# Performance work log

Measured on AMD Instinct MI355X. Metric: run time of the kernel, lower is better.

## Reference

```python
import jax, jax.numpy as jnp
import numpy as np

RRELU_SLOPE = (1.0 / 8.0 + 1.0 / 3.0) / 2.0  # F.rrelu eval mode
N_ENT, N_REL2, H, E, B, T = 20000, 460, 128, 400000, 1024, 8


def _lin(x, W, b):
    return x @ W.T + b  # torch nn.Linear convention


def _gru_cell(x, h, w_ih, w_hh, b_ih, b_hh):
    gi = x @ w_ih.T + b_ih
    gh = h @ w_hh.T + b_hh
    i_r, i_z, i_n = jnp.split(gi, 3, axis=1)
    h_r, h_z, h_n = jnp.split(gh, 3, axis=1)
    r = jax.nn.sigmoid(i_r + h_r)
    z = jax.nn.sigmoid(i_z + h_z)
    n = jnp.tanh(i_n + r * h_n)
    return (1.0 - z) * n + z * h


def setup_inputs() -> dict:
    key = jax.random.key(0)
    ks = jax.random.split(key, 24)
    s = 0.02
    inp = {
        'ent_emb': jax.random.normal(ks[0], (N_ENT, H), jnp.float32),
        'rel_emb': jax.random.normal(ks[1], (N_REL2, H), jnp.float32),
        'weight_neighbor': jax.random.normal(ks[2], (H, H), jnp.float32) * s,
        'loop_weight': jax.random.normal(ks[3], (H, H), jnp.float32) * s,
        'evolve_loop_weight': jax.random.normal(ks[4], (H, H), jnp.float32) * s,
        'w_ih': jax.random.normal(ks[5], (3 * H, H), jnp.float32) * s,
        'w_hh': jax.random.normal(ks[6], (3 * H, H), jnp.float32) * s,
        'b_ih': jnp.zeros((3 * H,), jnp.float32),
        'b_hh': jnp.zeros((3 * H,), jnp.float32),
        'W_map1': jax.random.normal(ks[7], (2 * H, H), jnp.float32) * s,
        'b_map1': jnp.zeros((2 * H,), jnp.float32),
        'W_map2': jax.random.normal(ks[8], (H, 2 * H), jnp.float32) * s,
        'b_map2': jnp.zeros((H,), jnp.float32),
        'W_h1': jax.random.normal(ks[9], (H, H), jnp.float32) * s,
        'b_h1': jnp.zeros((H,), jnp.float32),
        'W_h2': jax.random.normal(ks[10], (H, H), jnp.float32) * s,
        'b_h2': jnp.zeros((H,), jnp.float32),
        'W_align': jax.random.normal(ks[11], (H, H), jnp.float32) * s,
        'b_align': jnp.zeros((H,), jnp.float32),
        'W_attn': jax.random.normal(ks[12], (H, H), jnp.float32) * s,
        'b_attn': jnp.zeros((H,), jnp.float32),
    }
    u = jax.random.uniform(ks[13], (B, T * N_REL2), jnp.float32)
    mask = jax.random.uniform(ks[14], (B, T * N_REL2)) > 0.7  # sparse history
    inp['partial_embeding'] = u * mask
    inp['edge_src'] = jax.random.randint(ks[15], (E,), 0, N_ENT, jnp.int32)
    inp['edge_dst'] = jax.random.randint(ks[16], (E,), 0, N_ENT, jnp.int32)
    inp['edge_type'] = jax.random.randint(ks[17], (E,), 0, N_REL2, jnp.int32)
    sub = jax.random.randint(ks[18], (B,), 0, N_ENT, jnp.int32)
    rel = jax.random.randint(ks[19], (B,), 0, N_REL2, jnp.int32)
    obj = jax.random.randint(ks[20], (B,), 0, N_ENT, jnp.int32)
    inp['triples'] = jnp.stack([sub, rel, obj], axis=1)
    return inp


def reference(ent_emb, rel_emb, weight_neighbor, loop_weight, evolve_loop_weight,
              w_ih, w_hh, b_ih, b_hh, W_map1, b_map1, W_map2, b_map2,
              W_h1, b_h1, W_h2, b_h2, W_align, b_align, W_attn, b_attn,
              partial_embeding, edge_src, edge_dst, edge_type, triples):
    # ---- UnionRGCNLayer: gather-transform-scatter ----
    h = ent_emb
    msg = (h[edge_src] + rel_emb[edge_type]) @ weight_neighbor          # [E, H]
    agg = jax.ops.segment_sum(msg, edge_dst, num_segments=N_ENT)        # [N, H]
    deg = jax.ops.segment_sum(jnp.ones((edge_dst.shape[0],), h.dtype), edge_dst,
                              num_segments=N_ENT)
    norm = jnp.where(deg > 0, 1.0 / jnp.where(deg > 0, deg, 1.0), 0.0)[:, None]
    loop = jnp.where((deg > 0)[:, None], h @ loop_weight, h @ evolve_loop_weight)
    x = agg * norm + loop
    pre_emb = jnp.where(x >= 0, x, x * RRELU_SLOPE)                     # rrelu (eval)

    # ---- PathPredictor.forward_back ----
    mapped_rel = _lin(_lin(rel_emb, W_map1, b_map1), W_map2, b_map2)    # [2R, H]
    q_rel = mapped_rel[triples[:, 1]]                                   # [B, H]
    A = _lin(q_rel, W_attn, b_attn) @ mapped_rel.T                      # [B, 2R]
    hist = partial_embeding.reshape(B, T, N_REL2).transpose(1, 0, 2)    # [T, B, 2R]

    def step(gh, cur):
        attn = cur * A
        attn = jax.nn.softmax(jnp.where(attn == 0, -1e9, attn), axis=1)
        rel_path = attn @ mapped_rel                                    # [B, H]
        return _gru_cell(rel_path, gh, w_ih, w_hh, b_ih, b_hh), None

    gru_hidden, _ = jax.lax.scan(step, jnp.zeros((B, H), pre_emb.dtype), hist)
    predicted_hist = 0.1 * _lin(_lin(q_rel, W_h1, b_h1), W_h2, b_h2) + q_rel
    match_loss = jnp.mean((predicted_hist - gru_hidden) ** 2)

    # ---- forward_forth, distmult scoring ----
    gh2 = _gru_cell(q_rel, predicted_hist, w_ih, w_hh, b_ih, b_hh)      # [B, H]
    sub_emb = pre_emb[triples[:, 0]]
    aligned_all = _lin(pre_emb, W_align, b_align)                       # [N, H]
    score_ = (_lin(sub_emb, W_align, b_align) * gh2) @ aligned_all.T    # [B, N]
    score = jax.nn.sigmoid(score_)
    # BCE(score, one_hot(obj)) without materializing labels:
    logp = jax.nn.log_sigmoid(score_)
    log1mp = jax.nn.log_sigmoid(-score_)
    total = -jnp.sum(log1mp)
    rows = jnp.arange(B)
    total = total + jnp.sum(log1mp[rows, triples[:, 2]] - logp[rows, triples[:, 2]])
    path_loss = total / (B * N_ENT)
    return score, match_loss, path_loss
```

## Files before the change

kernel.cpp:

```cpp
#include <hip/hip_runtime.h>

typedef unsigned short u16;
typedef unsigned int u32;
typedef __attribute__((ext_vector_type(8))) short bf8v;
typedef __attribute__((ext_vector_type(4))) float f4v;

#define RRELU_SLOPE 0.22916666667f

__device__ inline float bf2f(u16 u){ unsigned int i = ((unsigned int)u) << 16; float f; __builtin_memcpy(&f, &i, 4); return f; }
__device__ inline u16 f2bf(float f){ unsigned int i; __builtin_memcpy(&i, &f, 4); unsigned int r = (i + 0x7fffu + ((i >> 16) & 1u)) >> 16; return (u16)r; }
__device__ inline float frcp(float x){ return __builtin_amdgcn_rcpf(x); }
__device__ inline float fsigm(float x){ return frcp(1.f + __expf(-x)); }
__device__ inline float ftanh(float x){ return 2.f * frcp(1.f + __expf(-2.f * x)) - 1.f; }

__global__ __launch_bounds__(256) void prep_k(
    const float* __restrict__ Wn, const float* __restrict__ Wl, const float* __restrict__ We,
    const float* __restrict__ wih, const float* __restrict__ whh,
    const float* __restrict__ m1, const float* __restrict__ m2,
    const float* __restrict__ h1, const float* __restrict__ h2,
    const float* __restrict__ attn, const float* __restrict__ alg, const float* __restrict__ rel,
    const float* __restrict__ ent, const float* __restrict__ bat, const float* __restrict__ bh1,
    u16* __restrict__ Bcat, u16* __restrict__ wihb, u16* __restrict__ whhb,
    u16* __restrict__ m1b, u16* __restrict__ m2b, u16* __restrict__ h1b, u16* __restrict__ h2b,
    u16* __restrict__ attnb, u16* __restrict__ algb, u16* __restrict__ relb,
    u16* __restrict__ entb, float* __restrict__ bias2)
{
    int id = blockIdx.x * 256 + threadIdx.x;
    if (id < 49152) {
        int n = id / 384, k = id % 384;
        float v = (k < 128) ? Wn[k*128 + n] : (k < 256 ? Wl[(k-128)*128 + n] : We[(k-256)*128 + n]);
        Bcat[id] = f2bf(v); return;
    }
    id -= 49152;
    if (id < 49152) { wihb[id] = f2bf(wih[id]); return; } id -= 49152;
    if (id < 49152) { whhb[id] = f2bf(whh[id]); return; } id -= 49152;
    if (id < 32768) { m1b[id]  = f2bf(m1[id]);  return; } id -= 32768;
    if (id < 32768) { m2b[id]  = f2bf(m2[id]);  return; } id -= 32768;
    if (id < 16384) { h1b[id]  = f2bf(h1[id]);  return; } id -= 16384;
    if (id < 16384) { h2b[id]  = f2bf(h2[id]);  return; } id -= 16384;
    if (id < 16384) { attnb[id]= f2bf(attn[id]);return; } id -= 16384;
    if (id < 16384) { algb[id] = f2bf(alg[id]); return; } id -= 16384;
    if (id < 58880) { relb[id] = f2bf(rel[id]); return; } id -= 58880;
    if (id < 2560000) { entb[id] = f2bf(ent[id]); return; } id -= 2560000;
    if (id < 256) { bias2[id] = (id < 128) ? bat[id] : bh1[id - 128]; }
}

__global__ __launch_bounds__(256) void hist_k(
    const int* __restrict__ dst, int* __restrict__ hist, int E)
{
    int e = blockIdx.x * 256 + threadIdx.x;
    if (e < E) atomicAdd(&hist[dst[e]], 1);
}

__global__ __launch_bounds__(1024) void scan_k(
    const int* __restrict__ hist, int* __restrict__ starts, int* __restrict__ cursor)
{
    __shared__ int part[1024];
    int t = threadIdx.x;
    int base = t * 20;
    int s = 0;
    for (int j = 0; j < 20; ++j) { int idx = base + j; if (idx < 20000) s += hist[idx]; }
    part[t] = s;
    __syncthreads();
    for (int off = 1; off < 1024; off <<= 1) {
        int v = (t >= off) ? part[t - off] : 0;
        __syncthreads();
        part[t] += v;
        __syncthreads();
    }
    int run = (t > 0) ? part[t - 1] : 0;
    for (int j = 0; j < 20; ++j) {
        int idx = base + j;
        if (idx < 20000) { starts[idx] = run; cursor[idx] = run; run += hist[idx]; }
    }
    if (t == 1023) starts[20000] = run;
}

__global__ __launch_bounds__(256) void scatter_k(
    const int* __restrict__ src, const int* __restrict__ dst, const int* __restrict__ typ,
    int* __restrict__ cursor, int2* __restrict__ spack, int E)
{
    int e = blockIdx.x * 256 + threadIdx.x;
    if (e >= E) return;
    int d = dst[e];
    int p = atomicAdd(&cursor[d], 1);
    spack[p] = make_int2(src[e], typ[e]);
}

__global__ __launch_bounds__(64) void agg_acat_k(
    const int2* __restrict__ spack, const int* __restrict__ starts,
    const u32* __restrict__ hb, const u32* __restrict__ rb, u32* __restrict__ Acat32)
{
    int i = blockIdx.x;
    int lane = threadIdx.x;
    int s0 = starts[i], s1 = starts[i + 1];
    float sx = 0.f, sy = 0.f;
    int e = s0;
    for (; e + 4 <= s1; e += 4) {
        int2 st0 = spack[e], st1 = spack[e+1], st2 = spack[e+2], st3 = spack[e+3];
        u32 a0 = hb[(long)st0.x * 64 + lane]; u32 r0 = rb[(long)st0.y * 64 + lane];
        u32 a1 = hb[(long)st1.x * 64 + lane]; u32 r1 = rb[(long)st1.y * 64 + lane];
        u32 a2 = hb[(long)st2.x * 64 + lane]; u32 r2 = rb[(long)st2.y * 64 + lane];
        u32 a3 = hb[(long)st3.x * 64 + lane]; u32 r3 = rb[(long)st3.y * 64 + lane];
        sx += bf2f((u16)(a0 & 0xffff)) + bf2f((u16)(r0 & 0xffff));
        sy += bf2f((u16)(a0 >> 16))    + bf2f((u16)(r0 >> 16));
        sx += bf2f((u16)(a1 & 0xffff)) + bf2f((u16)(r1 & 0xffff));
        sy += bf2f((u16)(a1 >> 16))    + bf2f((u16)(r1 >> 16));
        sx += bf2f((u16)(a2 & 0xffff)) + bf2f((u16)(r2 & 0xffff));
        sy += bf2f((u16)(a2 >> 16))    + bf2f((u16)(r2 >> 16));
        sx += bf2f((u16)(a3 & 0xffff)) + bf2f((u16)(r3 & 0xffff));
        sy += bf2f((u16)(a3 >> 16))    + bf2f((u16)(r3 >> 16));
    }
    for (; e < s1; ++e) {
        int2 st = spack[e];
        u32 a = hb[(long)st.x * 64 + lane];
        u32 r = rb[(long)st.y * 64 + lane];
        sx += bf2f((u16)(a & 0xffff)) + bf2f((u16)(r & 0xffff));
        sy += bf2f((u16)(a >> 16))    + bf2f((u16)(r >> 16));
    }
    bool has = s1 > s0;
    float nrm = has ? frcp((float)(s1 - s0)) : 0.f;
    u32 hv = hb[(long)i * 64 + lane];
    u32 agg = (u32)f2bf(sx * nrm) | ((u32)f2bf(sy * nrm) << 16);
    long o = (long)i * 192 + lane;
    Acat32[o]       = agg;
    Acat32[o + 64]  = has ? hv : 0u;
    Acat32[o + 128] = has ? 0u : hv;
}

__global__ __launch_bounds__(256) void gemm_nt(
    const u16* __restrict__ A, const u16* __restrict__ B, const float* __restrict__ bias,
    float* __restrict__ Cf, u16* __restrict__ Cbf, u16* __restrict__ CT,
    const u16* __restrict__ residb, const int* __restrict__ arows,
    int M, int N, int K, int lda, int ldb, int ldc, int ldct, int arow_stride,
    float rscale, int epi)
{
    int tid = threadIdx.x;
    int wave = tid >> 6, lane = tid & 63;
    int ln = lane & 15, q = lane >> 4;
    int bm = blockIdx.y * 64 + wave * 16;
    int bn = blockIdx.x * 64;
    int am = bm + ln; if (am >= M) am = M - 1;
    long ar = arows ? (long)arows[(long)am * arow_stride] : (long)am;
    const u16* Ap = A + ar * lda;
    int br[4];
#pragma unroll
    for (int nt = 0; nt < 4; ++nt) { int n = bn + nt*16 + ln; br[nt] = (n < N) ? n : (N - 1); }
    f4v acc[4] = {};
    for (int kc = 0; kc < K; kc += 32) {
        bf8v af = *(const bf8v*)(Ap + kc + q*8);
#pragma unroll
        for (int nt = 0; nt < 4; ++nt) {
            bf8v bv = *(const bf8v*)(B + (long)br[nt]*ldb + kc + q*8);
            acc[nt] = __builtin_amdgcn_mfma_f32_16x16x32_bf16(af, bv, acc[nt], 0, 0, 0);
        }
    }
#pragma unroll
    for (int nt = 0; nt < 4; ++nt) {
        int n = bn + nt*16 + ln;
        if (n >= N) continue;
        float bv = bias ? bias[n] : 0.f;
#pragma unroll
        for (int r = 0; r < 4; ++r) {
            int m = bm + q*4 + r;
            if (m >= M) continue;
            float v = acc[nt][r] + bv;
            if (epi == 1) v = (v >= 0.f) ? v : v * RRELU_SLOPE;
            if (residb)  v = rscale * v + bf2f(residb[(long)m*ldc + n]);
            long ci = (long)m*ldc + n;
            if (Cf)  Cf[ci]  = v;
            if (Cbf) Cbf[ci] = f2bf(v);
            if (CT)  CT[(long)n*ldct + m] = f2bf(v);
        }
    }
}

__global__ __launch_bounds__(256) void fuse_map_k(
    const u16* __restrict__ relb, const u16* __restrict__ m1b, const float* __restrict__ bm1,
    const u16* __restrict__ m2b, const float* __restrict__ bm2,
    u16* __restrict__ mapb, u16* __restrict__ mapT)
{
    __shared__ u16 t1l[4][16][264];
    int tid = threadIdx.x;
    int wave = tid >> 6, lane = tid & 63;
    int ln = lane & 15, q = lane >> 4;
    int base = blockIdx.x * 64 + wave * 16;
    int arow = base + ln; if (arow > 459) arow = 459;
    const u16* Ap = relb + arow * 128;
    f4v acc1[16] = {};
    for (int kc = 0; kc < 128; kc += 32) {
        bf8v af = *(const bf8v*)(Ap + kc + q*8);
#pragma unroll
        for (int nt = 0; nt < 16; ++nt) {
            bf8v bv = *(const bf8v*)(m1b + (nt*16 + ln)*128 + kc + q*8);
            acc1[nt] = __builtin_amdgcn_mfma_f32_16x16x32_bf16(af, bv, acc1[nt], 0, 0, 0);
        }
    }
#pragma unroll
    for (int nt = 0; nt < 16; ++nt) {
        int n = nt*16 + ln;
        float bv = bm1[n];
#pragma unroll
        for (int r = 0; r < 4; ++r)
            t1l[wave][q*4 + r][n] = f2bf(acc1[nt][r] + bv);
    }
    f4v acc2[8] = {};
    for (int kc = 0; kc < 256; kc += 32) {
        bf8v af = *(const bf8v*)&t1l[wave][ln][kc + q*8];
#pragma unroll
        for (int nt = 0; nt < 8; ++nt) {
            bf8v bv = *(const bf8v*)(m2b + (nt*16 + ln)*256 + kc + q*8);
            acc2[nt] = __builtin_amdgcn_mfma_f32_16x16x32_bf16(af, bv, acc2[nt], 0, 0, 0);
        }
    }
#pragma unroll
    for (int nt = 0; nt < 8; ++nt) {
        int n = nt*16 + ln;
        float bv = bm2[n];
#pragma unroll
        for (int r = 0; r < 4; ++r) {
            int m = base + q*4 + r;
            if (m < 460) {
                u16 hv = f2bf(acc2[nt][r] + bv);
                mapb[m*128 + n] = hv;
                mapT[n*480 + m] = hv;
            }
        }
    }
}

__global__ __launch_bounds__(256) void qrel_k(
    const u16* __restrict__ mapb, const int* __restrict__ trip,
    u16* __restrict__ qrelb, u16* __restrict__ X)
{
    int id = blockIdx.x * 256 + threadIdx.x;
    int b = id >> 7, k = id & 127;
    int r = trip[b*3 + 1];
    u16 v = mapb[r*128 + k];
    qrelb[id] = v;
    X[(long)(8192 + b)*128 + k] = v;
}

__global__ __launch_bounds__(256) void fuse_qt_k(
    const u16* __restrict__ qrelb, const u16* __restrict__ atb, const float* __restrict__ bias2,
    const u16* __restrict__ h2b, const float* __restrict__ bh2,
    u16* __restrict__ atq, float* __restrict__ pred)
{
    __shared__ u16 th1l[4][16][136];
    int tid = threadIdx.x;
    int wave = tid >> 6, lane = tid & 63;
    int ln = lane & 15, q = lane >> 4;
    int base = blockIdx.x * 64 + wave * 16;
    const u16* Ap = qrelb + (base + ln) * 128;
    f4v acc1[16] = {};
    for (int kc = 0; kc < 128; kc += 32) {
        bf8v af = *(const bf8v*)(Ap + kc + q*8);
#pragma unroll
        for (int nt = 0; nt < 16; ++nt) {
            bf8v bv = *(const bf8v*)(atb + (nt*16 + ln)*128 + kc + q*8);
            acc1[nt] = __builtin_amdgcn_mfma_f32_16x16x32_bf16(af, bv, acc1[nt], 0, 0, 0);
        }
    }
#pragma unroll
    for (int nt = 0; nt < 16; ++nt) {
        int n = nt*16 + ln;
        float bv = bias2[n];
#pragma unroll
        for (int r = 0; r < 4; ++r) {
            float x = acc1[nt][r] + bv;
            if (nt < 8) atq[(base + q*4 + r)*128 + n] = f2bf(x);
            else        th1l[wave][q*4 + r][n - 128] = f2bf(x);
        }
    }
    f4v acc2[8] = {};
    for (int kc = 0; kc < 128; kc += 32) {
        bf8v af = *(const bf8v*)&th1l[wave][ln][kc + q*8];
#pragma unroll
        for (int nt = 0; nt < 8; ++nt) {
            bf8v bv = *(const bf8v*)(h2b + (nt*16 + ln)*128 + kc + q*8);
            acc2[nt] = __builtin_amdgcn_mfma_f32_16x16x32_bf16(af, bv, acc2[nt], 0, 0, 0);
        }
    }
#pragma unroll
    for (int nt = 0; nt < 8; ++nt) {
        int n = nt*16 + ln;
        float bv = bh2[n];
#pragma unroll
        for (int r = 0; r < 4; ++r) {
            int m = base + q*4 + r;
            pred[(long)m*128 + n] = 0.1f * (acc2[nt][r] + bv) + bf2f(qrelb[(long)m*128 + n]);
        }
    }
}

__global__ __launch_bounds__(256) void smrp_k(
    const float* __restrict__ Amat, const float* __restrict__ part,
    const u16* __restrict__ mapT, u16* __restrict__ X)
{
    __shared__ u16 xls[32][488];
    int tid = threadIdx.x;
    int wave = tid >> 6, lane = tid & 63;
    int base = blockIdx.x * 32;
    int t = base >> 10, b0 = base & 1023;
    for (int j = 0; j < 8; ++j) {
        int rl = wave*8 + j;
        int b = b0 + rl;
        const float* arow = Amat + (long)b*460;
        const float* crow = part + (long)b*3680 + t*460;
        float v[8], e[8];
        float m = -1e30f;
#pragma unroll
        for (int i = 0; i < 8; ++i) {
            int r = i*64 + lane;
            if (r < 460) {
                float x = crow[r] * arow[r];
                x = (x == 0.f) ? -1e9f : x;
                v[i] = x; m = fmaxf(m, x);
            } else v[i] = -1e30f;
        }
#pragma unroll
        for (int off = 32; off; off >>= 1) m = fmaxf(m, __shfl_xor(m, off));
        float sum = 0.f;
#pragma unroll
        for (int i = 0; i < 8; ++i) {
            int r = i*64 + lane;
            e[i] = 0.f;
            if (r < 460) { e[i] = __expf(v[i] - m); sum += e[i]; }
        }
#pragma unroll
        for (int off = 32; off; off >>= 1) sum += __shfl_xor(sum, off);
        float inv = frcp(sum);
#pragma unroll
        for (int i = 0; i < 8; ++i) {
            int r = i*64 + lane;
            if (r < 460)      xls[rl][r] = f2bf(e[i] * inv);
            else if (r < 488) xls[rl][r] = 0;
        }
    }
    __syncthreads();
    int ln = lane & 15, q = lane >> 4;
    f4v acc[2][2] = {};
    for (int kc = 0; kc < 480; kc += 32) {
        bf8v a[2], bfr[2];
#pragma unroll
        for (int mt = 0; mt < 2; ++mt)
            a[mt] = *(const bf8v*)&xls[mt*16 + ln][kc + q*8];
#pragma unroll
        for (int nt = 0; nt < 2; ++nt)
            bfr[nt] = *(const bf8v*)(mapT + (wave*32 + nt*16 + ln)*480 + kc + q*8);
#pragma unroll
        for (int mt = 0; mt < 2; ++mt)
#pragma unroll
            for (int nt = 0; nt < 2; ++nt)
                acc[mt][nt] = __builtin_amdgcn_mfma_f32_16x16x32_bf16(a[mt], bfr[nt], acc[mt][nt], 0, 0, 0);
    }
#pragma unroll
    for (int mt = 0; mt < 2; ++mt)
#pragma unroll
    for (int nt = 0; nt < 2; ++nt) {
        int n = wave*32 + nt*16 + ln;
#pragma unroll
        for (int r = 0; r < 4; ++r) {
            int m = base + mt*16 + q*4 + r;
            X[(long)m*128 + n] = f2bf(acc[mt][nt][r]);
        }
    }
}

__global__ __launch_bounds__(256) void gru_k(
    const float* __restrict__ gi, const u16* __restrict__ whhb, const float* __restrict__ bhh,
    const float* __restrict__ pred, float* __restrict__ gh2, float* __restrict__ match_acc)
{
    __shared__ u16  hbf[16][136];
    __shared__ float hf [4][128];
    __shared__ float ghl[4][388];
    __shared__ float red[4];
    int tid = threadIdx.x;
    int wave = tid >> 6, lane = tid & 63;
    int ln = lane & 15, q = lane >> 4;
    int bb = blockIdx.x * 4;
    for (int i = tid; i < 16*136; i += 256) hbf[i/136][i%136] = 0;
    for (int i = tid; i < 4*128; i += 256) hf[i>>7][i&127] = 0.f;
    bf8v bfrag[6][4];
#pragma unroll
    for (int nt = 0; nt < 6; ++nt)
#pragma unroll
        for (int kc = 0; kc < 4; ++kc)
            bfrag[nt][kc] = *(const bf8v*)(whhb + (long)(wave*96 + nt*16 + ln)*128 + kc*32 + q*8);
    int k = tid & 127;
    float br = bhh[k], bz = bhh[128 + k], bn_ = bhh[256 + k];
    __syncthreads();
    float msum = 0.f;
    for (int t = 0; t <= 8; ++t) {
        float gr[2], gz[2], gn[2], pv[2];
        long girow0 = (t < 8) ? ((long)t*1024 + bb) : (8192 + bb);
#pragma unroll
        for (int it = 0; it < 2; ++it) {
            int m = it*2 + (tid >> 7);
            const float* gp = gi + (girow0 + m)*384;
            gr[it] = gp[k]; gz[it] = gp[128 + k]; gn[it] = gp[256 + k];
            pv[it] = (t >= 7) ? pred[(long)(bb + m)*128 + k] : 0.f;
        }
        if (t == 8) {
#pragma unroll
            for (int it = 0; it < 2; ++it) {
                int m = it*2 + (tid >> 7);
                hf[m][k] = pv[it]; hbf[m][k] = f2bf(pv[it]);
            }
            __syncthreads();
        }
        f4v acc[6] = {};
#pragma unroll
        for (int kc = 0; kc < 4; ++kc) {
            bf8v af = *(const bf8v*)&hbf[ln][kc*32 + q*8];
#pragma unroll
            for (int nt = 0; nt < 6; ++nt)
                acc[nt] = __builtin_amdgcn_mfma_f32_16x16x32_bf16(af, bfrag[nt][kc], acc[nt], 0, 0, 0);
        }
        if (q == 0) {
#pragma unroll
            for (int nt = 0; nt < 6; ++nt)
#pragma unroll
                for (int r = 0; r < 4; ++r)
                    ghl[r][wave*96 + nt*16 + ln] = acc[nt][r];
        }
        __syncthreads();
#pragma unroll
        for (int it = 0; it < 2; ++it) {
            int m = it*2 + (tid >> 7);
            float rr = fsigm(gr[it] + ghl[m][k] + br);
            float zz = fsigm(gz[it] + ghl[m][128 + k] + bz);
            float nn = ftanh(gn[it] + rr * (ghl[m][256 + k] + bn_));
            float hn = (1.f - zz) * nn + zz * hf[m][k];
            if (t == 7) { float d = pv[it] - hn; msum += d*d; }
            if (t == 8) { gh2[(long)(bb + m)*128 + k] = hn; }
            else        { hf[m][k] = hn; hbf[m][k] = f2bf(hn); }
        }
        __syncthreads();
    }
#pragma unroll
    for (int off = 32; off; off >>= 1) msum += __shfl_down(msum, off);
    if (lane == 0) red[wave] = msum;
    __syncthreads();
    if (tid == 0) atomicAdd(match_acc, red[0] + red[1] + red[2] + red[3]);
}

__global__ __launch_bounds__(128) void vo_k(
    const float* __restrict__ subl, const float* __restrict__ gh2,
    const u16* __restrict__ AL, const int* __restrict__ trip,
    u16* __restrict__ V, float* __restrict__ obj_acc)
{
    int b = blockIdx.x, k = threadIdx.x;
    u16 vb = f2bf(subl[b*128 + k] * gh2[b*128 + k]);
    V[b*128 + k] = vb;
    int obj = trip[b*3 + 2];
    float s = bf2f(vb) * bf2f(AL[(long)obj*128 + k]);
#pragma unroll
    for (int off = 32; off; off >>= 1) s += __shfl_down(s, off);
    __shared__ float red2[2];
    if ((k & 63) == 0) red2[k >> 6] = s;
    __syncthreads();
    if (k == 0) atomicAdd(obj_acc, -(red2[0] + red2[1]));
}

__global__ __launch_bounds__(512) void score_k(
    const u16* __restrict__ V, const u16* __restrict__ AL,
    float* __restrict__ out, float* __restrict__ sp_acc, int N)
{
    __shared__ float stage[8][2048];
    int tid = threadIdx.x;
    int wave = tid >> 6, lane = tid & 63;
    int ln = lane & 15, q = lane >> 4;
    int bm = blockIdx.y * 128 + (wave >> 2) * 64;
    int bn = blockIdx.x * 128 + (wave & 3) * 32;
    bool valid = bn < N;
    int br[2];
#pragma unroll
    for (int nt = 0; nt < 2; ++nt) { int n = bn + nt*16 + ln; br[nt] = (n < N) ? n : (N - 1); }
    f4v acc[4][2] = {};
    for (int kc = 0; kc < 128; kc += 32) {
        bf8v a[4], b[2];
#pragma unroll
        for (int mt = 0; mt < 4; ++mt)
            a[mt] = *(const bf8v*)(V + (long)(bm + mt*16 + ln)*128 + kc + q*8);
#pragma unroll
        for (int nt = 0; nt < 2; ++nt)
            b[nt] = *(const bf8v*)(AL + (long)br[nt]*128 + kc + q*8);
#pragma unroll
        for (int mt = 0; mt < 4; ++mt)
#pragma unroll
            for (int nt = 0; nt < 2; ++nt)
                acc[mt][nt] = __builtin_amdgcn_mfma_f32_16x16x32_bf16(a[mt], b[nt], acc[mt][nt], 0, 0, 0);
    }
    float lsum = 0.f;
    float* st = stage[wave];
#pragma unroll
    for (int mt = 0; mt < 4; ++mt)
#pragma unroll
    for (int nt = 0; nt < 2; ++nt)
#pragma unroll
    for (int r = 0; r < 4; ++r) {
        float s = acc[mt][nt][r];
        float e = __expf(-fabsf(s));
        float d = 1.f + e;
        float inv = frcp(d);
        st[(mt*16 + q*4 + r)*32 + nt*16 + ln] = (s >= 0.f) ? inv : e * inv;
        lsum += fmaxf(s, 0.f) + __logf(d);
    }
    if (!valid) lsum = 0.f;
    if (valid) {
        int row0 = lane >> 3, c4 = (lane & 7) << 2;
#pragma unroll
        for (int i = 0; i < 8; ++i) {
            int row = i*8 + row0;
            f4v vv = *(const f4v*)&st[row*32 + c4];
            __builtin_nontemporal_store(vv, (f4v*)&out[(long)(bm + row)*N + bn + c4]);
        }
    }
#pragma unroll
    for (int off = 32; off; off >>= 1) lsum += __shfl_xor(lsum, off);
    __shared__ float red[8];
    if (lane == 0) red[wave] = lsum;
    __syncthreads();
    if (tid == 0) {
        float tsum = 0.f;
#pragma unroll
        for (int w = 0; w < 8; ++w) tsum += red[w];
        atomicAdd(sp_acc, tsum);
    }
}

__global__ void final_k(const float* __restrict__ acc, float* __restrict__ out)
{
    out[20480000] = acc[0] / (1024.f * 128.f);
    out[20480001] = (acc[1] + acc[2]) / (1024.f * 20000.f);
}

extern "C" void kernel_launch(void* const* d_in, const int* in_sizes, int n_in,
                              void* d_out, int out_size, void* d_ws, size_t ws_size,
                              hipStream_t stream)
{
    const float* ent  = (const float*)d_in[0];
    const float* rel  = (const float*)d_in[1];
    const float* Wn   = (const float*)d_in[2];
    const float* Wl   = (const float*)d_in[3];
    const float* We   = (const float*)d_in[4];
    const float* wih  = (const float*)d_in[5];
    const float* whh  = (const float*)d_in[6];
    const float* b_ih = (const float*)d_in[7];
    const float* b_hh = (const float*)d_in[8];
    const float* Wm1  = (const float*)d_in[9];
    const float* bm1  = (const float*)d_in[10];
    const float* Wm2  = (const float*)d_in[11];
    const float* bm2  = (const float*)d_in[12];
    const float* Wh1  = (const float*)d_in[13];
    const float* bh1  = (const float*)d_in[14];
    const float* Wh2  = (const float*)d_in[15];
    const float* bh2  = (const float*)d_in[16];
    const float* Wal  = (const float*)d_in[17];
    const float* bal  = (const float*)d_in[18];
    const float* Wat  = (const float*)d_in[19];
    const float* bat  = (const float*)d_in[20];
    const float* part = (const float*)d_in[21];
    const int* esrc   = (const int*)d_in[22];
    const int* edst   = (const int*)d_in[23];
    const int* etyp   = (const int*)d_in[24];
    const int* trip   = (const int*)d_in[25];
    float* out = (float*)d_out;
    const int E = in_sizes[22];

    char* ws = (char*)d_ws;
    size_t off = 0;
    auto alloc = [&](size_t bytes) { size_t o = off; off = (off + bytes + 255) & ~(size_t)255; return o; };

    size_t o_acc   = alloc(256);
    size_t o_hist  = alloc(20000 * 4);
    size_t o_mapT  = alloc(128 * 480 * 2);
    size_t zend = off;
    size_t o_starts= alloc(20004 * 4);
    size_t o_cur   = alloc(20000 * 4);
    size_t o_spack = alloc((size_t)E * 8);
    size_t o_entb  = alloc((size_t)20000 * 128 * 2);
    size_t o_acat  = alloc((size_t)20000 * 384 * 2);
    size_t o_pre   = alloc((size_t)20000 * 128 * 2);
    size_t o_aln   = alloc((size_t)20000 * 128 * 2);
    size_t o_bcat  = alloc(128 * 384 * 2);
    size_t o_wih   = alloc(384 * 128 * 2);
    size_t o_whh   = alloc(384 * 128 * 2);
    size_t o_m1    = alloc(256 * 128 * 2);
    size_t o_m2    = alloc(128 * 256 * 2);
    size_t o_ath   = alloc(2 * 128 * 128 * 2);
    size_t o_h2    = alloc(128 * 128 * 2);
    size_t o_al    = alloc(128 * 128 * 2);
    size_t o_rel   = alloc(460 * 128 * 2);
    size_t o_map   = alloc(460 * 128 * 2);
    size_t o_qrel  = alloc(1024 * 128 * 2);
    size_t o_atq   = alloc(1024 * 128 * 2);
    size_t o_b2    = alloc(256 * 4);
    size_t o_pred  = alloc(1024 * 128 * 4);
    size_t o_amat  = alloc((size_t)1024 * 460 * 4);
    size_t o_X     = alloc((size_t)9216 * 128 * 2);
    size_t o_gi    = alloc((size_t)9216 * 384 * 4);
    size_t o_subl  = alloc(1024 * 128 * 4);
    size_t o_gh2   = alloc(1024 * 128 * 4);
    size_t o_V     = alloc(1024 * 128 * 2);

    float* accp  = (float*)(ws + o_acc);
    int* histp   = (int*)(ws + o_hist);
    u16* mapT    = (u16*)(ws + o_mapT);
    int* startsp = (int*)(ws + o_starts);
    int* curp    = (int*)(ws + o_cur);
    int2* spack  = (int2*)(ws + o_spack);
    u16* entb    = (u16*)(ws + o_entb);
    u16* acat    = (u16*)(ws + o_acat);
    u16* preb    = (u16*)(ws + o_pre);
    u16* alnb    = (u16*)(ws + o_aln);
    u16* bcat    = (u16*)(ws + o_bcat);
    u16* wihb    = (u16*)(ws + o_wih);
    u16* whhb    = (u16*)(ws + o_whh);
    u16* m1b     = (u16*)(ws + o_m1);
    u16* m2b     = (u16*)(ws + o_m2);
    u16* atb     = (u16*)(ws + o_ath);
    u16* h1b     = atb + 128 * 128;
    u16* h2b     = (u16*)(ws + o_h2);
    u16* alb     = (u16*)(ws + o_al);
    u16* relb    = (u16*)(ws + o_rel);
    u16* mapb    = (u16*)(ws + o_map);
    u16* qrelb   = (u16*)(ws + o_qrel);
    u16* atqb    = (u16*)(ws + o_atq);
    float* bias2 = (float*)(ws + o_b2);
    float* predf = (float*)(ws + o_pred);
    float* amat  = (float*)(ws + o_amat);
    u16* Xb      = (u16*)(ws + o_X);
    float* gif   = (float*)(ws + o_gi);
    float* subl  = (float*)(ws + o_subl);
    float* gh2f  = (float*)(ws + o_gh2);
    u16* Vb      = (u16*)(ws + o_V);

    hipMemsetAsync(ws, 0, zend, stream);

    prep_k<<<11319, 256, 0, stream>>>(Wn, Wl, We, wih, whh, Wm1, Wm2, Wh1, Wh2, Wat, Wal, rel,
                                      ent, bat, bh1,
                                      bcat, wihb, whhb, m1b, m2b, h1b, h2b, atb, alb, relb,
                                      entb, bias2);

    int eb = (E + 255) / 256;
    hist_k<<<eb, 256, 0, stream>>>(edst, histp, E);
    scan_k<<<1, 1024, 0, stream>>>(histp, startsp, curp);
    scatter_k<<<eb, 256, 0, stream>>>(esrc, edst, etyp, curp, spack, E);
    agg_acat_k<<<20000, 64, 0, stream>>>(spack, startsp, (const u32*)entb, (const u32*)relb, (u32*)acat);

    gemm_nt<<<dim3(2, 313), 256, 0, stream>>>(acat, bcat, nullptr, nullptr, preb, nullptr, nullptr, nullptr,
                                              20000, 128, 384, 384, 384, 128, 0, 0, 0.f, 1);
    gemm_nt<<<dim3(2, 313), 256, 0, stream>>>(preb, alb, bal, nullptr, alnb, nullptr, nullptr, nullptr,
                                              20000, 128, 128, 128, 128, 128, 0, 0, 0.f, 0);

    fuse_map_k<<<8, 256, 0, stream>>>(relb, m1b, bm1, m2b, bm2, mapb, mapT);

    qrel_k<<<512, 256, 0, stream>>>(mapb, trip, qrelb, Xb);

    fuse_qt_k<<<16, 256, 0, stream>>>(qrelb, atb, bias2, h2b, bh2, atqb, predf);

    gemm_nt<<<dim3(8, 16), 256, 0, stream>>>(atqb, mapb, nullptr, amat, nullptr, nullptr, nullptr, nullptr,
                                             1024, 460, 128, 128, 128, 460, 0, 0, 0.f, 0);

    smrp_k<<<256, 256, 0, stream>>>(amat, part, mapT, Xb);

    gemm_nt<<<dim3(6, 144), 256, 0, stream>>>(Xb, wihb, b_ih, gif, nullptr, nullptr, nullptr, nullptr,
                                              9216, 384, 128, 128, 128, 384, 0, 0, 0.f, 0);
    gemm_nt<<<dim3(2, 16), 256, 0, stream>>>(preb, alb, bal, subl, nullptr, nullptr, nullptr, trip,
                                             1024, 128, 128, 128, 128, 128, 0, 3, 0.f, 0);

    gru_k<<<256, 256, 0, stream>>>(gif, whhb, b_hh, predf, gh2f, accp + 0);

    vo_k<<<1024, 128, 0, stream>>>(subl, gh2f, alnb, trip, Vb, accp + 2);

    score_k<<<dim3(157, 8), 512, 0, stream>>>(Vb, alnb, out, accp + 1, 20000);

    final_k<<<1, 1, 0, stream>>>(accp, out);

    (void)in_sizes; (void)n_in; (void)out_size; (void)ws_size;
}
```

Measured before the change: 470.1 us.

## Fuse input-gate GEMM, vo and final into GRU; merge small kernels

Computes the GRU input projection inside the recurrent kernel from the bf16 X rows using register-resident W_ih fragments. This removes the 9216x384 fp32 gi buffer and its separate GEMM. The vo and final reductions are folded into gru_k and into score_k through a last-block counter, the histogram moves into prep_k, and qrel_k is folded into fuse_qt_k. smrp_k is regrouped so each block stages four Amat rows in shared memory across all timesteps. The cost is more registers and MFMA work on the serial GRU path, plus occupancy limited to one block per SM.

```diff
diff --git a/kernel.cpp b/kernel.cpp
--- a/kernel.cpp
+++ b/kernel.cpp
@@ -20,10 +20,11 @@
     const float* __restrict__ h1, const float* __restrict__ h2,
     const float* __restrict__ attn, const float* __restrict__ alg, const float* __restrict__ rel,
     const float* __restrict__ ent, const float* __restrict__ bat, const float* __restrict__ bh1,
+    const int* __restrict__ edst, int E,
     u16* __restrict__ Bcat, u16* __restrict__ wihb, u16* __restrict__ whhb,
     u16* __restrict__ m1b, u16* __restrict__ m2b, u16* __restrict__ h1b, u16* __restrict__ h2b,
     u16* __restrict__ attnb, u16* __restrict__ algb, u16* __restrict__ relb,
-    u16* __restrict__ entb, float* __restrict__ bias2)
+    u16* __restrict__ entb, float* __restrict__ bias2, int* __restrict__ hist)
 {
     int id = blockIdx.x * 256 + threadIdx.x;
     if (id < 49152) {
@@ -42,14 +43,8 @@
     if (id < 16384) { algb[id] = f2bf(alg[id]); return; } id -= 16384;
     if (id < 58880) { relb[id] = f2bf(rel[id]); return; } id -= 58880;
     if (id < 2560000) { entb[id] = f2bf(ent[id]); return; } id -= 2560000;
-    if (id < 256) { bias2[id] = (id < 128) ? bat[id] : bh1[id - 128]; }
-}
-
-__global__ __launch_bounds__(256) void hist_k(
-    const int* __restrict__ dst, int* __restrict__ hist, int E)
-{
-    int e = blockIdx.x * 256 + threadIdx.x;
-    if (e < E) atomicAdd(&hist[dst[e]], 1);
+    if (id < 256) { bias2[id] = (id < 128) ? bat[id] : bh1[id - 128]; return; } id -= 256;
+    if (id < E) atomicAdd(&hist[edst[id]], 1);
 }
 
 __global__ __launch_bounds__(1024) void scan_k(
@@ -229,29 +224,22 @@
     }
 }
 
-__global__ __launch_bounds__(256) void qrel_k(
+__global__ __launch_bounds__(256) void fuse_qt_k(
     const u16* __restrict__ mapb, const int* __restrict__ trip,
-    u16* __restrict__ qrelb, u16* __restrict__ X)
-{
-    int id = blockIdx.x * 256 + threadIdx.x;
-    int b = id >> 7, k = id & 127;
-    int r = trip[b*3 + 1];
-    u16 v = mapb[r*128 + k];
-    qrelb[id] = v;
-    X[(long)(8192 + b)*128 + k] = v;
-}
-
-__global__ __launch_bounds__(256) void fuse_qt_k(
-    const u16* __restrict__ qrelb, const u16* __restrict__ atb, const float* __restrict__ bias2,
+    const u16* __restrict__ atb, const float* __restrict__ bias2,
     const u16* __restrict__ h2b, const float* __restrict__ bh2,
-    u16* __restrict__ atq, float* __restrict__ pred)
+    u16* __restrict__ atq, float* __restrict__ pred, u16* __restrict__ X)
 {
     __shared__ u16 th1l[4][16][136];
     int tid = threadIdx.x;
     int wave = tid >> 6, lane = tid & 63;
     int ln = lane & 15, q = lane >> 4;
     int base = blockIdx.x * 64 + wave * 16;
-    const u16* Ap = qrelb + (base + ln) * 128;
+    int ar = trip[(base + ln)*3 + 1];
+    const u16* Ap = mapb + ar * 128;
+    int rm_[4];
+#pragma unroll
+    for (int r = 0; r < 4; ++r) rm_[r] = trip[(base + q*4 + r)*3 + 1];
     f4v acc1[16] = {};
     for (int kc = 0; kc < 128; kc += 32) {
         bf8v af = *(const bf8v*)(Ap + kc + q*8);
@@ -267,9 +255,12 @@
         float bv = bias2[n];
 #pragma unroll
         for (int r = 0; r < 4; ++r) {
+            int m = base + q*4 + r;
             float x = acc1[nt][r] + bv;
-            if (nt < 8) atq[(base + q*4 + r)*128 + n] = f2bf(x);
-            else        th1l[wave][q*4 + r][n - 128] = f2bf(x);
+            if (nt < 8) {
+                atq[m*128 + n] = f2bf(x);
+                X[(long)(8192 + m)*128 + n] = mapb[rm_[r]*128 + n];
+            } else th1l[wave][q*4 + r][n - 128] = f2bf(x);
         }
     }
     f4v acc2[8] = {};
@@ -288,7 +279,7 @@
 #pragma unroll
         for (int r = 0; r < 4; ++r) {
             int m = base + q*4 + r;
-            pred[(long)m*128 + n] = 0.1f * (acc2[nt][r] + bv) + bf2f(qrelb[(long)m*128 + n]);
+            pred[(long)m*128 + n] = 0.1f * (acc2[nt][r] + bv) + bf2f(mapb[rm_[r]*128 + n]);
         }
     }
 }
@@ -298,22 +289,24 @@
     const u16* __restrict__ mapT, u16* __restrict__ X)
 {
     __shared__ u16 xls[32][488];
+    __shared__ float asl[4][464];
     int tid = threadIdx.x;
     int wave = tid >> 6, lane = tid & 63;
-    int base = blockIdx.x * 32;
-    int t = base >> 10, b0 = base & 1023;
+    int b0 = blockIdx.x * 4;
+    for (int i = tid; i < 4*460; i += 256)
+        asl[i/460][i%460] = Amat[(long)(b0 + i/460)*460 + i%460];
+    __syncthreads();
     for (int j = 0; j < 8; ++j) {
         int rl = wave*8 + j;
-        int b = b0 + rl;
-        const float* arow = Amat + (long)b*460;
-        const float* crow = part + (long)b*3680 + t*460;
+        int t = rl >> 2, db = rl & 3;
+        const float* crow = part + (long)(b0 + db)*3680 + t*460;
         float v[8], e[8];
         float m = -1e30f;
 #pragma unroll
         for (int i = 0; i < 8; ++i) {
             int r = i*64 + lane;
             if (r < 460) {
-                float x = crow[r] * arow[r];
+                float x = crow[r] * asl[db][r];
                 x = (x == 0.f) ? -1e9f : x;
                 v[i] = x; m = fmaxf(m, x);
             } else v[i] = -1e30f;
@@ -361,44 +354,50 @@
         int n = wave*32 + nt*16 + ln;
 #pragma unroll
         for (int r = 0; r < 4; ++r) {
-            int m = base + mt*16 + q*4 + r;
-            X[(long)m*128 + n] = f2bf(acc[mt][nt][r]);
-        }
-    }
-}
-
-__global__ __launch_bounds__(256) void gru_k(
-    const float* __restrict__ gi, const u16* __restrict__ whhb, const float* __restrict__ bhh,
-    const float* __restrict__ pred, float* __restrict__ gh2, float* __restrict__ match_acc)
+            int rl = mt*16 + q*4 + r;
+            long m = (long)(rl >> 2)*1024 + b0 + (rl & 3);
+            X[m*128 + n] = f2bf(acc[mt][nt][r]);
+        }
+    }
+}
+
+__global__ __launch_bounds__(256, 1) void gru_k(
+    const u16* __restrict__ X, const u16* __restrict__ wihb, const float* __restrict__ bih,
+    const u16* __restrict__ whhb, const float* __restrict__ bhh,
+    const float* __restrict__ pred, const float* __restrict__ subl,
+    const u16* __restrict__ AL, const int* __restrict__ trip,
+    u16* __restrict__ V, float* __restrict__ accp)
 {
     __shared__ u16  hbf[16][136];
     __shared__ float hf [4][128];
     __shared__ float ghl[4][388];
-    __shared__ float red[4];
+    __shared__ float gil[4][388];
+    __shared__ float redm[4], redo[4];
     int tid = threadIdx.x;
     int wave = tid >> 6, lane = tid & 63;
     int ln = lane & 15, q = lane >> 4;
     int bb = blockIdx.x * 4;
     for (int i = tid; i < 16*136; i += 256) hbf[i/136][i%136] = 0;
     for (int i = tid; i < 4*128; i += 256) hf[i>>7][i&127] = 0.f;
-    bf8v bfrag[6][4];
+    bf8v bfrag[6][4], wfrag[6][4];
 #pragma unroll
     for (int nt = 0; nt < 6; ++nt)
 #pragma unroll
-        for (int kc = 0; kc < 4; ++kc)
+        for (int kc = 0; kc < 4; ++kc) {
             bfrag[nt][kc] = *(const bf8v*)(whhb + (long)(wave*96 + nt*16 + ln)*128 + kc*32 + q*8);
+            wfrag[nt][kc] = *(const bf8v*)(wihb + (long)(wave*96 + nt*16 + ln)*128 + kc*32 + q*8);
+        }
     int k = tid & 127;
-    float br = bhh[k], bz = bhh[128 + k], bn_ = bhh[256 + k];
+    float cr = bih[k] + bhh[k];
+    float cz = bih[128 + k] + bhh[128 + k];
+    float bin_ = bih[256 + k], bhn = bhh[256 + k];
     __syncthreads();
-    float msum = 0.f;
+    float msum = 0.f, osum = 0.f;
     for (int t = 0; t <= 8; ++t) {
-        float gr[2], gz[2], gn[2], pv[2];
-        long girow0 = (t < 8) ? ((long)t*1024 + bb) : (8192 + bb);
+        float pv[2];
 #pragma unroll
         for (int it = 0; it < 2; ++it) {
             int m = it*2 + (tid >> 7);
-            const float* gp = gi + (girow0 + m)*384;
-            gr[it] = gp[k]; gz[it] = gp[128 + k]; gn[it] = gp[256 + k];
             pv[it] = (t >= 7) ? pred[(long)(bb + m)*128 + k] : 0.f;
         }
         if (t == 8) {
@@ -409,63 +408,60 @@
             }
             __syncthreads();
         }
+        long xr0 = (t < 8) ? ((long)t*1024 + bb) : (long)(8192 + bb);
+        const u16* Xp = X + (xr0 + (ln & 3))*128;
+        f4v gacc[6] = {};
         f4v acc[6] = {};
 #pragma unroll
         for (int kc = 0; kc < 4; ++kc) {
+            bf8v xf = *(const bf8v*)(Xp + kc*32 + q*8);
             bf8v af = *(const bf8v*)&hbf[ln][kc*32 + q*8];
 #pragma unroll
+            for (int nt = 0; nt < 6; ++nt) {
+                gacc[nt] = __builtin_amdgcn_mfma_f32_16x16x32_bf16(xf, wfrag[nt][kc], gacc[nt], 0, 0, 0);
+                acc[nt]  = __builtin_amdgcn_mfma_f32_16x16x32_bf16(af, bfrag[nt][kc], acc[nt],  0, 0, 0);
+            }
+        }
+        if (q == 0) {
+#pragma unroll
             for (int nt = 0; nt < 6; ++nt)
-                acc[nt] = __builtin_amdgcn_mfma_f32_16x16x32_bf16(af, bfrag[nt][kc], acc[nt], 0, 0, 0);
-        }
-        if (q == 0) {
-#pragma unroll
-            for (int nt = 0; nt < 6; ++nt)
-#pragma unroll
-                for (int r = 0; r < 4; ++r)
+#pragma unroll
+                for (int r = 0; r < 4; ++r) {
                     ghl[r][wave*96 + nt*16 + ln] = acc[nt][r];
+                    gil[r][wave*96 + nt*16 + ln] = gacc[nt][r];
+                }
         }
         __syncthreads();
 #pragma unroll
         for (int it = 0; it < 2; ++it) {
             int m = it*2 + (tid >> 7);
-            float rr = fsigm(gr[it] + ghl[m][k] + br);
-            float zz = fsigm(gz[it] + ghl[m][128 + k] + bz);
-            float nn = ftanh(gn[it] + rr * (ghl[m][256 + k] + bn_));
+            float rr = fsigm(gil[m][k] + ghl[m][k] + cr);
+            float zz = fsigm(gil[m][128 + k] + ghl[m][128 + k] + cz);
+            float nn = ftanh(gil[m][256 + k] + bin_ + rr * (ghl[m][256 + k] + bhn));
             float hn = (1.f - zz) * nn + zz * hf[m][k];
             if (t == 7) { float d = pv[it] - hn; msum += d*d; }
-            if (t == 8) { gh2[(long)(bb + m)*128 + k] = hn; }
-            else        { hf[m][k] = hn; hbf[m][k] = f2bf(hn); }
+            if (t == 8) {
+                u16 vb = f2bf(subl[(long)(bb + m)*128 + k] * hn);
+                V[(long)(bb + m)*128 + k] = vb;
+                int obj = trip[(bb + m)*3 + 2];
+                osum += bf2f(vb) * bf2f(AL[(long)obj*128 + k]);
+            } else { hf[m][k] = hn; hbf[m][k] = f2bf(hn); }
         }
         __syncthreads();
     }
 #pragma unroll
-    for (int off = 32; off; off >>= 1) msum += __shfl_down(msum, off);
-    if (lane == 0) red[wave] = msum;
+    for (int off = 32; off; off >>= 1) { msum += __shfl_down(msum, off); osum += __shfl_down(osum, off); }
+    if (lane == 0) { redm[wave] = msum; redo[wave] = osum; }
     __syncthreads();
-    if (tid == 0) atomicAdd(match_acc, red[0] + red[1] + red[2] + red[3]);
-}
-
-__global__ __launch_bounds__(128) void vo_k(
-    const float* __restrict__ subl, const float* __restrict__ gh2,
-    const u16* __restrict__ AL, const int* __restrict__ trip,
-    u16* __restrict__ V, float* __restrict__ obj_acc)
-{
-    int b = blockIdx.x, k = threadIdx.x;
-    u16 vb = f2bf(subl[b*128 + k] * gh2[b*128 + k]);
-    V[b*128 + k] = vb;
-    int obj = trip[b*3 + 2];
-    float s = bf2f(vb) * bf2f(AL[(long)obj*128 + k]);
-#pragma unroll
-    for (int off = 32; off; off >>= 1) s += __shfl_down(s, off);
-    __shared__ float red2[2];
-    if ((k & 63) == 0) red2[k >> 6] = s;
-    __syncthreads();
-    if (k == 0) atomicAdd(obj_acc, -(red2[0] + red2[1]));
+    if (tid == 0) {
+        atomicAdd(accp + 0, redm[0] + redm[1] + redm[2] + redm[3]);
+        atomicAdd(accp + 2, -(redo[0] + redo[1] + redo[2] + redo[3]));
+    }
 }
 
 __global__ __launch_bounds__(512) void score_k(
     const u16* __restrict__ V, const u16* __restrict__ AL,
-    float* __restrict__ out, float* __restrict__ sp_acc, int N)
+    float* __restrict__ out, float* __restrict__ accp, int N)
 {
     __shared__ float stage[8][2048];
     int tid = threadIdx.x;
@@ -526,14 +522,18 @@
         float tsum = 0.f;
 #pragma unroll
         for (int w = 0; w < 8; ++w) tsum += red[w];
-        atomicAdd(sp_acc, tsum);
-    }
-}
-
-__global__ void final_k(const float* __restrict__ acc, float* __restrict__ out)
-{
-    out[20480000] = acc[0] / (1024.f * 128.f);
-    out[20480001] = (acc[1] + acc[2]) / (1024.f * 20000.f);
+        atomicAdd(accp + 1, tsum);
+        __threadfence();
+        u32* cnt = (u32*)accp + 3;
+        u32 c = atomicAdd(cnt, 1u);
+        if (c == gridDim.x * gridDim.y - 1) {
+            float mm = atomicAdd(accp + 0, 0.f);
+            float sp = atomicAdd(accp + 1, 0.f);
+            float ob = atomicAdd(accp + 2, 0.f);
+            out[20480000] = mm / (1024.f * 128.f);
+            out[20480001] = (sp + ob) / (1024.f * 20000.f);
+        }
+    }
 }
 
 extern "C" void kernel_launch(void* const* d_in, const int* in_sizes, int n_in,
@@ -594,15 +594,12 @@
     size_t o_al    = alloc(128 * 128 * 2);
     size_t o_rel   = alloc(460 * 128 * 2);
     size_t o_map   = alloc(460 * 128 * 2);
-    size_t o_qrel  = alloc(1024 * 128 * 2);
     size_t o_atq   = alloc(1024 * 128 * 2);
     size_t o_b2    = alloc(256 * 4);
     size_t o_pred  = alloc(1024 * 128 * 4);
     size_t o_amat  = alloc((size_t)1024 * 460 * 4);
     size_t o_X     = alloc((size_t)9216 * 128 * 2);
-    size_t o_gi    = alloc((size_t)9216 * 384 * 4);
     size_t o_subl  = alloc(1024 * 128 * 4);
-    size_t o_gh2   = alloc(1024 * 128 * 4);
     size_t o_V     = alloc(1024 * 128 * 2);
 
     float* accp  = (float*)(ws + o_acc);
@@ -626,27 +623,25 @@
     u16* alb     = (u16*)(ws + o_al);
     u16* relb    = (u16*)(ws + o_rel);
     u16* mapb    = (u16*)(ws + o_map);
-    u16* qrelb   = (u16*)(ws + o_qrel);
     u16* atqb    = (u16*)(ws + o_atq);
     float* bias2 = (float*)(ws + o_b2);
     float* predf = (float*)(ws + o_pred);
     float* amat  = (float*)(ws + o_amat);
     u16* Xb      = (u16*)(ws + o_X);
-    float* gif   = (float*)(ws + o_gi);
     float* subl  = (float*)(ws + o_subl);
-    float* gh2f  = (float*)(ws + o_gh2);
     u16* Vb      = (u16*)(ws + o_V);
 
     hipMemsetAsync(ws, 0, zend, stream);
 
-    prep_k<<<11319, 256, 0, stream>>>(Wn, Wl, We, wih, whh, Wm1, Wm2, Wh1, Wh2, Wat, Wal, rel,
-                                      ent, bat, bh1,
-                                      bcat, wihb, whhb, m1b, m2b, h1b, h2b, atb, alb, relb,
-                                      entb, bias2);
-
+    int ptot = 2897664 + E;
+    prep_k<<<(ptot + 255) / 256, 256, 0, stream>>>(
+        Wn, Wl, We, wih, whh, Wm1, Wm2, Wh1, Wh2, Wat, Wal, rel,
+        ent, bat, bh1, edst, E,
+        bcat, wihb, whhb, m1b, m2b, h1b, h2b, atb, alb, relb,
+        entb, bias2, histp);
+
+    scan_k<<<1, 1024, 0, stream>>>(histp, startsp, curp);
     int eb = (E + 255) / 256;
-    hist_k<<<eb, 256, 0, stream>>>(edst, histp, E);
-    scan_k<<<1, 1024, 0, stream>>>(histp, startsp, curp);
     scatter_k<<<eb, 256, 0, stream>>>(esrc, edst, etyp, curp, spack, E);
     agg_acat_k<<<20000, 64, 0, stream>>>(spack, startsp, (const u32*)entb, (const u32*)relb, (u32*)acat);
 
@@ -657,27 +652,19 @@
 
     fuse_map_k<<<8, 256, 0, stream>>>(relb, m1b, bm1, m2b, bm2, mapb, mapT);
 
-    qrel_k<<<512, 256, 0, stream>>>(mapb, trip, qrelb, Xb);
-
-    fuse_qt_k<<<16, 256, 0, stream>>>(qrelb, atb, bias2, h2b, bh2, atqb, predf);
+    fuse_qt_k<<<16, 256, 0, stream>>>(mapb, trip, atb, bias2, h2b, bh2, atqb, predf, Xb);
 
     gemm_nt<<<dim3(8, 16), 256, 0, stream>>>(atqb, mapb, nullptr, amat, nullptr, nullptr, nullptr, nullptr,
                                              1024, 460, 128, 128, 128, 460, 0, 0, 0.f, 0);
 
     smrp_k<<<256, 256, 0, stream>>>(amat, part, mapT, Xb);
 
-    gemm_nt<<<dim3(6, 144), 256, 0, stream>>>(Xb, wihb, b_ih, gif, nullptr, nullptr, nullptr, nullptr,
-                                              9216, 384, 128, 128, 128, 384, 0, 0, 0.f, 0);
     gemm_nt<<<dim3(2, 16), 256, 0, stream>>>(preb, alb, bal, subl, nullptr, nullptr, nullptr, trip,
                                              1024, 128, 128, 128, 128, 128, 0, 3, 0.f, 0);
 
-    gru_k<<<256, 256, 0, stream>>>(gif, whhb, b_hh, predf, gh2f, accp + 0);
-
-    vo_k<<<1024, 128, 0, stream>>>(subl, gh2f, alnb, trip, Vb, accp + 2);
-
-    score_k<<<dim3(157, 8), 512, 0, stream>>>(Vb, alnb, out, accp + 1, 20000);
-
-    final_k<<<1, 1, 0, stream>>>(accp, out);
+    gru_k<<<256, 256, 0, stream>>>(Xb, wihb, b_ih, whhb, b_hh, predf, subl, alnb, trip, Vb, accp);
+
+    score_k<<<dim3(157, 8), 512, 0, stream>>>(Vb, alnb, out, accp, 20000);
 
     (void)in_sizes; (void)n_in; (void)out_size; (void)ws_size;
 }
```

Result: no change. 476.5 us (+1.4%).
